# Kernel tuning notes

Hardware: AMD Instinct MI355X
Metric: run time of the kernel (lower is better)

## Reference

```python
import jax, jax.numpy as jnp
import numpy as np

NUM_WORDS = 256  # max word index + 1 (sentinel row NUM_WORDS used to drop non-first-occurrence scatters)


def setup_inputs() -> dict:
    key = jax.random.key(0)
    ks = jax.random.split(key, 8)
    B, S, H, R, D, C = 16, 512, 768, 8, 512, 27
    hidden_states = jax.random.normal(ks[0], (B, S, H), jnp.float32)
    word_ids = jnp.sort(jax.random.randint(ks[1], (B, S), 0, NUM_WORDS), axis=-1)
    relations_positions = jax.random.randint(ks[2], (B, R), 0, S)
    w_rel = jax.random.normal(ks[3], (H,), jnp.float32) / np.sqrt(H).astype(np.float32)
    b_rel = jnp.zeros((1,), jnp.float32)
    w1 = jax.random.normal(ks[4], (2 * H, D), jnp.float32) / np.sqrt(2 * H).astype(np.float32)
    b1 = jnp.zeros((D,), jnp.float32)
    w2 = jax.random.normal(ks[5], (D, C), jnp.float32) / np.sqrt(D).astype(np.float32)
    b2 = jnp.zeros((C,), jnp.float32)
    return dict(hidden_states=hidden_states, word_ids=word_ids,
                relations_positions=relations_positions,
                w_rel=w_rel, b_rel=b_rel, w1=w1, b1=b1, w2=w2, b2=b2)


def reference(hidden_states, word_ids, relations_positions, w_rel, b_rel, w1, b1, w2, b2):
    B, S, H = hidden_states.shape
    # relational logits: Linear(H, 1).squeeze(-1)  -> [B, S]
    rel_logits = jnp.einsum('bsh,h->bs', hidden_states, w_rel) + b_rel

    # first_hidden_states[i, w] = hidden_states[i, j] at the FIRST token j of word w
    # (torch loop keys on word_id != prev_word_id; word_ids are monotone per row)
    first_occ = jnp.concatenate(
        [jnp.ones((B, 1), bool), word_ids[:, 1:] != word_ids[:, :-1]], axis=1)
    tgt = jnp.where(first_occ, word_ids, NUM_WORDS)  # route non-first tokens to sentinel row
    batch_idx = jnp.arange(B)[:, None]
    first_hidden = (jnp.zeros((B, NUM_WORDS + 1, H), hidden_states.dtype)
                    .at[batch_idx, tgt].set(hidden_states))[:, :NUM_WORDS]  # [B, W, H]

    # gather relation token embeddings -> [B, R, H]
    rel_hidden = jnp.take_along_axis(
        hidden_states, relations_positions[:, :, None], axis=1)

    # concat([word_embed, rel_embed]) @ w1 == word_embed @ w1[:H] + rel_embed @ w1[H:]
    h_word = jnp.einsum('bwh,hd->bwd', first_hidden, w1[:H])   # [B, W, D]
    h_rel = jnp.einsum('brh,hd->brd', rel_hidden, w1[H:])      # [B, R, D]
    hmid = jax.nn.relu(h_word[:, None, :, :] + h_rel[:, :, None, :] + b1)  # [B, R, W, D]
    role_logits = jnp.einsum('brwd,dc->brwc', hmid, w2) + b2   # [B, R, W, C]

    return rel_logits, role_logits
```

## Files before the change

### kernel.cpp

```cpp
#include <hip/hip_runtime.h>
#include <hip/hip_bf16.h>

#define BB 16
#define SS 512
#define HH 768
#define RR 8
#define DD 512
#define CC 27
#define WW 256

typedef __attribute__((ext_vector_type(8))) short short8;
typedef __attribute__((ext_vector_type(4))) float f32x4;

union PKu { unsigned short us[8]; uint4 u4; short8 s8; };

__device__ __forceinline__ unsigned short f32_to_bf16_rne(float v) {
    unsigned int u = __float_as_uint(v);
    unsigned int r = u + 0x7fffu + ((u >> 16) & 1u);
    return (unsigned short)(r >> 16);
}
__device__ __forceinline__ float bf16_to_f32(unsigned short u) {
    return __uint_as_float(((unsigned int)u) << 16);
}

__device__ __forceinline__ void glds16(const void* g, void* l) {
    __builtin_amdgcn_global_load_lds(
        (const __attribute__((address_space(1))) unsigned int*)g,
        (__attribute__((address_space(3))) unsigned int*)l, 16, 0, 0);
}


__global__ __launch_bounds__(256) void k_front(
    const float* __restrict__ hidden, const int* __restrict__ word_ids,
    const int* __restrict__ relpos, const float4* __restrict__ wrel4,
    const float* __restrict__ b_rel, const float* __restrict__ w1,
    const float* __restrict__ w2, float* __restrict__ out0,
    unsigned short* __restrict__ first_hidden,
    unsigned short* __restrict__ rel_hidden,
    unsigned short* __restrict__ w1t, unsigned short* __restrict__ w2t) {
    int bid = blockIdx.x, t = threadIdx.x;
    if (bid < 2048) {
        int lane = t & 63;
        int row = bid * 4 + (t >> 6);
        const float4* hid4 = (const float4*)hidden + (size_t)row * (HH / 4);
        float4 v[3];
        float acc = 0.f;
#pragma unroll
        for (int j = 0; j < 3; ++j) {
            v[j] = hid4[j * 64 + lane];
            float4 w = wrel4[j * 64 + lane];
            acc += v[j].x * w.x + v[j].y * w.y + v[j].z * w.z + v[j].w * w.w;
        }
#pragma unroll
        for (int off = 32; off > 0; off >>= 1) acc += __shfl_xor(acc, off, 64);
        if (lane == 0) out0[row] = acc + b_rel[0];
        int wid = word_ids[row];
        int s = row & (SS - 1);
        int prev = (s == 0) ? -1 : word_ids[row - 1];
        if (wid != prev) {
            int b = row >> 9;
            unsigned short* dst = first_hidden + (size_t)(b * WW + wid) * HH;
#pragma unroll
            for (int j = 0; j < 3; ++j) {
                union { unsigned short us[4]; uint2 u2; } pk;
                pk.us[0] = f32_to_bf16_rne(v[j].x);
                pk.us[1] = f32_to_bf16_rne(v[j].y);
                pk.us[2] = f32_to_bf16_rne(v[j].z);
                pk.us[3] = f32_to_bf16_rne(v[j].w);
                *(uint2*)(dst + j * 256 + lane * 4) = pk.u2;
            }
        }
        return;
    }
    int x = bid - 2048;
    if (x < 192) {
        __shared__ unsigned short tile[64][72];
        int kt = x >> 3, nt = x & 7;
        int i = t >> 2, j4 = (t & 3) * 16;
        const float* src = w1 + (size_t)(kt * 64 + i) * DD + nt * 64 + j4;
#pragma unroll
        for (int v = 0; v < 4; ++v) {
            float4 f = *(const float4*)(src + v * 4);
            tile[i][j4 + v * 4 + 0] = f32_to_bf16_rne(f.x);
            tile[i][j4 + v * 4 + 1] = f32_to_bf16_rne(f.y);
            tile[i][j4 + v * 4 + 2] = f32_to_bf16_rne(f.z);
            tile[i][j4 + v * 4 + 3] = f32_to_bf16_rne(f.w);
        }
        __syncthreads();
        int jj = t >> 2, cb = (t & 3) * 16;
        union { unsigned short us[16]; uint4 u4[2]; } ov;
#pragma unroll
        for (int v = 0; v < 16; ++v) ov.us[v] = tile[cb + v][jj];
        unsigned short* dst = w1t + (size_t)(nt * 64 + jj) * (2 * HH) + kt * 64 + cb;
        *(uint4*)(dst) = ov.u4[0];
        *(uint4*)(dst + 8) = ov.u4[1];
    } else if (x == 192) {
        for (int idx = t; idx < 32 * DD; idx += 256) {
            int n = idx >> 9, k = idx & (DD - 1);
            float v = (n < CC) ? w2[(size_t)k * CC + n] : 0.f;
            w2t[n * DD + k] = f32_to_bf16_rne(v);
        }
    } else {
        __shared__ int pres[WW];
        int b = x - 193;
        pres[t] = 0;
        __syncthreads();
        for (int s = t; s < SS; s += 256) pres[word_ids[b * SS + s]] = 1;
        __syncthreads();
        if (!pres[t]) {
            uint4 z = {0u, 0u, 0u, 0u};
            unsigned short* dst = first_hidden + (size_t)(b * WW + t) * HH;
#pragma unroll 4
            for (int c = 0; c < 96; ++c) *(uint4*)(dst + c * 8) = z;
        }
        for (int idx = t; idx < 1024; idx += 256) {
            int rr = idx >> 7, c = idx & 127;
            if (c < 96) {
                int pos = relpos[b * RR + rr];
                const float* srow = hidden + (size_t)(b * SS + pos) * HH + c * 8;
                PKu pk;
#pragma unroll
                for (int e = 0; e < 8; ++e) pk.us[e] = f32_to_bf16_rne(srow[e]);
                *(uint4*)(rel_hidden + (size_t)(b * RR + rr) * HH + c * 8) = pk.u4;
            }
        }
    }
}

__global__ __launch_bounds__(256) void k_gemm(
    const unsigned short* __restrict__ first_hidden,
    const unsigned short* __restrict__ rel_hidden,
    const unsigned short* __restrict__ w1t,
    unsigned short* __restrict__ h_word, unsigned short* __restrict__ h_rel) {
    __shared__ __align__(16) unsigned char a_s[32768];
    __shared__ __align__(16) unsigned char b_s[32768];
    int nt = blockIdx.x;
    int mt = blockIdx.y;
    const unsigned short* A;
    unsigned short* C;
    int kbase, m0;
    if (mt < 64) { A = first_hidden; C = h_word; kbase = 0;  m0 = mt * 64; }
    else         { A = rel_hidden;   C = h_rel;  kbase = HH; m0 = (mt - 64) * 64; }
    int t = threadIdx.x;
    int wv = t >> 6, lane = t & 63;
    int wr = wv >> 1, wc = wv & 1;
    int q = lane >> 4, r = lane & 15;

    const unsigned char* aP[4];
    const unsigned char* bP[4];
    unsigned lofs[4];
#pragma unroll
    for (int j = 0; j < 4; ++j) {
        int ci = j * 256 + t;
        int row = ci >> 4, ch = ci & 15;
        int sc = ch ^ (row & 7);
        aP[j] = (const unsigned char*)A + (size_t)(m0 + row) * (HH * 2) + sc * 16;
        bP[j] = (const unsigned char*)w1t + (size_t)(nt * 64 + row) * (2 * HH * 2)
                + (size_t)kbase * 2 + sc * 16;
        lofs[j] = ci * 16;
    }
    f32x4 acc[2][2];
#pragma unroll
    for (int mi = 0; mi < 2; ++mi)
#pragma unroll
        for (int ni = 0; ni < 2; ++ni) acc[mi][ni] = (f32x4){0.f, 0.f, 0.f, 0.f};

#pragma unroll
    for (int j = 0; j < 4; ++j) glds16(aP[j], a_s + lofs[j]);
#pragma unroll
    for (int j = 0; j < 4; ++j) glds16(bP[j], b_s + lofs[j]);
    __syncthreads();

#pragma unroll
    for (int kt = 0; kt < 6; ++kt) {
        if (kt < 5) {
            unsigned nb = ((kt + 1) & 1) * 16384;
#pragma unroll
            for (int j = 0; j < 4; ++j) glds16(aP[j] + (kt + 1) * 256, a_s + nb + lofs[j]);
#pragma unroll
            for (int j = 0; j < 4; ++j) glds16(bP[j] + (kt + 1) * 256, b_s + nb + lofs[j]);
        }
        unsigned bo = (kt & 1) * 16384;
#pragma unroll
        for (int ks = 0; ks < 4; ++ks) {
            int c = ks * 4 + q;
            short8 bfr[2];
#pragma unroll
            for (int ni = 0; ni < 2; ++ni) {
                int row = wc * 32 + ni * 16 + r;
                bfr[ni] = *(const short8*)(b_s + bo + row * 256 + ((c ^ (row & 7)) << 4));
            }
#pragma unroll
            for (int mi = 0; mi < 2; ++mi) {
                int row = wr * 32 + mi * 16 + r;
                short8 af = *(const short8*)(a_s + bo + row * 256 + ((c ^ (row & 7)) << 4));
                acc[mi][0] = __builtin_amdgcn_mfma_f32_16x16x32_bf16(
                    af, bfr[0], acc[mi][0], 0, 0, 0);
                acc[mi][1] = __builtin_amdgcn_mfma_f32_16x16x32_bf16(
                    af, bfr[1], acc[mi][1], 0, 0, 0);
            }
        }
        __syncthreads();
    }
#pragma unroll
    for (int mi = 0; mi < 2; ++mi) {
        int m = m0 + wr * 32 + mi * 16 + q * 4;
#pragma unroll
        for (int ni = 0; ni < 2; ++ni) {
            int n = nt * 64 + wc * 32 + ni * 16 + r;
#pragma unroll
            for (int reg = 0; reg < 4; ++reg)
                C[(size_t)(m + reg) * DD + n] = f32_to_bf16_rne(acc[mi][ni][reg]);
        }
    }
}

__global__ __launch_bounds__(512) void k_role(
    const unsigned short* __restrict__ h_word, const unsigned short* __restrict__ h_rel,
    const unsigned short* __restrict__ w2t, const float* __restrict__ b1,
    const float* __restrict__ b2, float* __restrict__ out_role) {
    int wt = blockIdx.x;
    int b  = blockIdx.y;
    int t  = threadIdx.x;
    __shared__ __align__(16) unsigned char hw_s[32768];
    __shared__ float hr_s[RR][DD];
    __shared__ __align__(16) unsigned char w2_s[32768];
    {
        int wl = t >> 5;
        int cb = (t & 31) * 4;
        const unsigned short* srcr = h_word + (size_t)(b * WW + wt * 16 + wl) * DD;
        unsigned wlx = (wl & 7) << 4;
#pragma unroll
        for (int i = 0; i < 4; ++i) {
            int c = cb + i;
            uint2 hv = *(const uint2*)(srcr + c * 4);
            float4 bv = *(const float4*)(b1 + c * 4);
            float4 o;
            o.x = bf16_to_f32((unsigned short)(hv.x & 0xffffu)) + bv.x;
            o.y = bf16_to_f32((unsigned short)(hv.x >> 16)) + bv.y;
            o.z = bf16_to_f32((unsigned short)(hv.y & 0xffffu)) + bv.z;
            o.w = bf16_to_f32((unsigned short)(hv.y >> 16)) + bv.w;
            *(float4*)(hw_s + wl * 2048 + ((unsigned)(c * 16) ^ wlx)) = o;
        }
    }
    {
        int rr = t >> 6, cc = (t & 63) * 8;
        PKu hv;
        hv.u4 = *(const uint4*)(h_rel + (size_t)(b * RR + rr) * DD + cc);
        float4 o0, o1;
        o0.x = bf16_to_f32(hv.us[0]); o0.y = bf16_to_f32(hv.us[1]);
        o0.z = bf16_to_f32(hv.us[2]); o0.w = bf16_to_f32(hv.us[3]);
        o1.x = bf16_to_f32(hv.us[4]); o1.y = bf16_to_f32(hv.us[5]);
        o1.z = bf16_to_f32(hv.us[6]); o1.w = bf16_to_f32(hv.us[7]);
        *(float4*)&hr_s[rr][cc]     = o0;
        *(float4*)&hr_s[rr][cc + 4] = o1;
    }
    {
        int n = t >> 4, cb = (t & 15) * 4;
        unsigned nx = (n & 7) << 4;
        const unsigned short* srcw = w2t + n * DD + cb * 8;
#pragma unroll
        for (int i = 0; i < 4; ++i)
            *(uint4*)(w2_s + n * 1024 + ((unsigned)((cb + i) * 16) ^ nx)) =
                *(const uint4*)(srcw + i * 8);
    }
    __syncthreads();
    int wv = t >> 6, lane = t & 63, q = lane >> 4, wl = lane & 15;
    int rr = wv;
    unsigned wlx = (wl & 7) << 4;
    f32x4 acc[2];
#pragma unroll
    for (int ni = 0; ni < 2; ++ni) acc[ni] = (f32x4){0.f, 0.f, 0.f, 0.f};

    for (int ks = 0; ks < DD / 32; ++ks) {
        int k0 = ks * 32;
        short8 bfr[2];
#pragma unroll
        for (int ni = 0; ni < 2; ++ni) {
            int n = ni * 16 + wl;
            bfr[ni] = *(const short8*)(w2_s + n * 1024 +
                        ((unsigned)((4 * ks + q) * 16) ^ wlx));
        }
        int c0 = 8 * ks + 2 * q;
        float4 f0 = *(const float4*)(hw_s + wl * 2048 + ((unsigned)(c0 * 16) ^ wlx));
        float4 f1 = *(const float4*)(hw_s + wl * 2048 + ((unsigned)((c0 + 1) * 16) ^ wlx));
        const float* hrp = &hr_s[rr][k0 + 8 * q];
        float4 h0 = *(const float4*)(hrp);
        float4 h1 = *(const float4*)(hrp + 4);
        PKu pk;
        pk.us[0] = f32_to_bf16_rne(fmaxf(f0.x + h0.x, 0.f));
        pk.us[1] = f32_to_bf16_rne(fmaxf(f0.y + h0.y, 0.f));
        pk.us[2] = f32_to_bf16_rne(fmaxf(f0.z + h0.z, 0.f));
        pk.us[3] = f32_to_bf16_rne(fmaxf(f0.w + h0.w, 0.f));
        pk.us[4] = f32_to_bf16_rne(fmaxf(f1.x + h1.x, 0.f));
        pk.us[5] = f32_to_bf16_rne(fmaxf(f1.y + h1.y, 0.f));
        pk.us[6] = f32_to_bf16_rne(fmaxf(f1.z + h1.z, 0.f));
        pk.us[7] = f32_to_bf16_rne(fmaxf(f1.w + h1.w, 0.f));
#pragma unroll
        for (int ni = 0; ni < 2; ++ni)
            acc[ni] = __builtin_amdgcn_mfma_f32_16x16x32_bf16(
                pk.s8, bfr[ni], acc[ni], 0, 0, 0);
    }
#pragma unroll
    for (int ni = 0; ni < 2; ++ni) {
        int c = ni * 16 + wl;
        if (c < CC) {
#pragma unroll
            for (int reg = 0; reg < 4; ++reg) {
                int wg = wt * 16 + 4 * q + reg;
                out_role[(size_t)((b * RR + rr) * WW + wg) * CC + c] =
                    acc[ni][reg] + b2[c];
            }
        }
    }
}

extern "C" void kernel_launch(void* const* d_in, const int* in_sizes, int n_in,
                              void* d_out, int out_size, void* d_ws, size_t ws_size,
                              hipStream_t stream) {
    const float* hidden   = (const float*)d_in[0];
    const int*   word_ids = (const int*)d_in[1];
    const int*   relpos   = (const int*)d_in[2];
    const float* w_rel    = (const float*)d_in[3];
    const float* b_rel    = (const float*)d_in[4];
    const float* w1       = (const float*)d_in[5];
    const float* b1       = (const float*)d_in[6];
    const float* w2       = (const float*)d_in[7];
    const float* b2       = (const float*)d_in[8];

    float* out0 = (float*)d_out;
    float* out1 = out0 + BB * SS;

    unsigned short* first_hidden = (unsigned short*)d_ws;
    unsigned short* rel_hidden   = (unsigned short*)((char*)d_ws + 6291456);
    unsigned short* w1t          = (unsigned short*)((char*)d_ws + 6488064);
    unsigned short* w2t          = (unsigned short*)((char*)d_ws + 8060928);
    unsigned short* h_word       = (unsigned short*)((char*)d_ws + 8093696);
    unsigned short* h_rel        = (unsigned short*)((char*)d_ws + 12288000);

    k_front<<<2048 + 209, 256, 0, stream>>>(
        hidden, word_ids, relpos, (const float4*)w_rel, b_rel, w1, w2,
        out0, first_hidden, rel_hidden, w1t, w2t);
    k_gemm<<<dim3(8, 66), 256, 0, stream>>>(
        first_hidden, rel_hidden, w1t, h_word, h_rel);
    k_role<<<dim3(WW / 16, BB), 512, 0, stream>>>(h_word, h_rel, w2t, b1, b2, out1);
}
```

Measured before the change: 46.52 us.

## Enlarge GEMM M-tile, fold b1 into GEMM epilogue, async-load role tiles

The word-projection GEMM now uses 128-row M tiles with a 64-wide K step. This halves the grid and doubles A-tile reuse of each B tile. The b1 bias is added in the GEMM epilogue instead of in k_role, so k_role can keep h_word as bf16 in shared memory and stage it and w2 with direct global-to-LDS loads rather than converting through registers. The trade-off is fewer blocks (264), which may underfill the GPU, and twice as many K iterations with more syncs.

```diff
diff --git a/kernel.cpp b/kernel.cpp
--- a/kernel.cpp
+++ b/kernel.cpp
@@ -130,70 +130,83 @@
 __global__ __launch_bounds__(256) void k_gemm(
     const unsigned short* __restrict__ first_hidden,
     const unsigned short* __restrict__ rel_hidden,
-    const unsigned short* __restrict__ w1t,
+    const unsigned short* __restrict__ w1t, const float* __restrict__ b1,
     unsigned short* __restrict__ h_word, unsigned short* __restrict__ h_rel) {
     __shared__ __align__(16) unsigned char a_s[32768];
-    __shared__ __align__(16) unsigned char b_s[32768];
+    __shared__ __align__(16) unsigned char b_s[16384];
     int nt = blockIdx.x;
     int mt = blockIdx.y;
-    const unsigned short* A;
-    unsigned short* C;
-    int kbase, m0;
-    if (mt < 64) { A = first_hidden; C = h_word; kbase = 0;  m0 = mt * 64; }
-    else         { A = rel_hidden;   C = h_rel;  kbase = HH; m0 = (mt - 64) * 64; }
+    bool isw = (mt < 32);
+    const unsigned short* A = isw ? first_hidden : rel_hidden;
+    unsigned short* C = isw ? h_word : h_rel;
+    int kbase = isw ? 0 : HH;
+    int m0 = isw ? mt * 128 : 0;
     int t = threadIdx.x;
     int wv = t >> 6, lane = t & 63;
     int wr = wv >> 1, wc = wv & 1;
     int q = lane >> 4, r = lane & 15;
 
     const unsigned char* aP[4];
-    const unsigned char* bP[4];
-    unsigned lofs[4];
+    const unsigned char* bP[2];
+    unsigned lofa[4], lofb[2];
 #pragma unroll
     for (int j = 0; j < 4; ++j) {
         int ci = j * 256 + t;
-        int row = ci >> 4, ch = ci & 15;
+        int row = ci >> 3, ch = ci & 7;
         int sc = ch ^ (row & 7);
         aP[j] = (const unsigned char*)A + (size_t)(m0 + row) * (HH * 2) + sc * 16;
+        lofa[j] = ci * 16;
+    }
+#pragma unroll
+    for (int j = 0; j < 2; ++j) {
+        int ci = j * 256 + t;
+        int row = ci >> 3, ch = ci & 7;
+        int sc = ch ^ (row & 7);
         bP[j] = (const unsigned char*)w1t + (size_t)(nt * 64 + row) * (2 * HH * 2)
                 + (size_t)kbase * 2 + sc * 16;
-        lofs[j] = ci * 16;
-    }
-    f32x4 acc[2][2];
-#pragma unroll
-    for (int mi = 0; mi < 2; ++mi)
+        lofb[j] = ci * 16;
+    }
+    int arow[4], brow[2];
+#pragma unroll
+    for (int mi = 0; mi < 4; ++mi) arow[mi] = wr * 64 + mi * 16 + r;
+#pragma unroll
+    for (int ni = 0; ni < 2; ++ni) brow[ni] = wc * 32 + ni * 16 + r;
+
+    f32x4 acc[4][2];
+#pragma unroll
+    for (int mi = 0; mi < 4; ++mi)
 #pragma unroll
         for (int ni = 0; ni < 2; ++ni) acc[mi][ni] = (f32x4){0.f, 0.f, 0.f, 0.f};
 
 #pragma unroll
-    for (int j = 0; j < 4; ++j) glds16(aP[j], a_s + lofs[j]);
-#pragma unroll
-    for (int j = 0; j < 4; ++j) glds16(bP[j], b_s + lofs[j]);
+    for (int j = 0; j < 4; ++j) glds16(aP[j], a_s + lofa[j]);
+#pragma unroll
+    for (int j = 0; j < 2; ++j) glds16(bP[j], b_s + lofb[j]);
     __syncthreads();
 
-#pragma unroll
-    for (int kt = 0; kt < 6; ++kt) {
-        if (kt < 5) {
-            unsigned nb = ((kt + 1) & 1) * 16384;
-#pragma unroll
-            for (int j = 0; j < 4; ++j) glds16(aP[j] + (kt + 1) * 256, a_s + nb + lofs[j]);
-#pragma unroll
-            for (int j = 0; j < 4; ++j) glds16(bP[j] + (kt + 1) * 256, b_s + nb + lofs[j]);
-        }
-        unsigned bo = (kt & 1) * 16384;
-#pragma unroll
-        for (int ks = 0; ks < 4; ++ks) {
+    for (int kt = 0; kt < 12; ++kt) {
+        if (kt < 11) {
+            unsigned na = ((kt + 1) & 1) * 16384;
+            unsigned nb = ((kt + 1) & 1) * 8192;
+#pragma unroll
+            for (int j = 0; j < 4; ++j) glds16(aP[j] + (kt + 1) * 128, a_s + na + lofa[j]);
+#pragma unroll
+            for (int j = 0; j < 2; ++j) glds16(bP[j] + (kt + 1) * 128, b_s + nb + lofb[j]);
+        }
+        unsigned ba = (kt & 1) * 16384;
+        unsigned bb = (kt & 1) * 8192;
+#pragma unroll
+        for (int ks = 0; ks < 2; ++ks) {
             int c = ks * 4 + q;
             short8 bfr[2];
 #pragma unroll
-            for (int ni = 0; ni < 2; ++ni) {
-                int row = wc * 32 + ni * 16 + r;
-                bfr[ni] = *(const short8*)(b_s + bo + row * 256 + ((c ^ (row & 7)) << 4));
-            }
-#pragma unroll
-            for (int mi = 0; mi < 2; ++mi) {
-                int row = wr * 32 + mi * 16 + r;
-                short8 af = *(const short8*)(a_s + bo + row * 256 + ((c ^ (row & 7)) << 4));
+            for (int ni = 0; ni < 2; ++ni)
+                bfr[ni] = *(const short8*)(b_s + bb + brow[ni] * 128 +
+                            ((c ^ (brow[ni] & 7)) << 4));
+#pragma unroll
+            for (int mi = 0; mi < 4; ++mi) {
+                short8 af = *(const short8*)(a_s + ba + arow[mi] * 128 +
+                            ((c ^ (arow[mi] & 7)) << 4));
                 acc[mi][0] = __builtin_amdgcn_mfma_f32_16x16x32_bf16(
                     af, bfr[0], acc[mi][0], 0, 0, 0);
                 acc[mi][1] = __builtin_amdgcn_mfma_f32_16x16x32_bf16(
@@ -202,100 +215,97 @@
         }
         __syncthreads();
     }
-#pragma unroll
-    for (int mi = 0; mi < 2; ++mi) {
-        int m = m0 + wr * 32 + mi * 16 + q * 4;
+    float bias[2];
+#pragma unroll
+    for (int ni = 0; ni < 2; ++ni) {
+        int n = nt * 64 + wc * 32 + ni * 16 + r;
+        bias[ni] = isw ? b1[n] : 0.f;
+    }
+#pragma unroll
+    for (int mi = 0; mi < 4; ++mi) {
+        int m = m0 + wr * 64 + mi * 16 + q * 4;
 #pragma unroll
         for (int ni = 0; ni < 2; ++ni) {
             int n = nt * 64 + wc * 32 + ni * 16 + r;
 #pragma unroll
             for (int reg = 0; reg < 4; ++reg)
-                C[(size_t)(m + reg) * DD + n] = f32_to_bf16_rne(acc[mi][ni][reg]);
+                C[(size_t)(m + reg) * DD + n] =
+                    f32_to_bf16_rne(acc[mi][ni][reg] + bias[ni]);
         }
     }
 }
 
 __global__ __launch_bounds__(512) void k_role(
     const unsigned short* __restrict__ h_word, const unsigned short* __restrict__ h_rel,
-    const unsigned short* __restrict__ w2t, const float* __restrict__ b1,
-    const float* __restrict__ b2, float* __restrict__ out_role) {
+    const unsigned short* __restrict__ w2t, const float* __restrict__ b2,
+    float* __restrict__ out_role) {
     int wt = blockIdx.x;
     int b  = blockIdx.y;
     int t  = threadIdx.x;
-    __shared__ __align__(16) unsigned char hw_s[32768];
+    __shared__ __align__(16) unsigned char hw_s[16384];
     __shared__ float hr_s[RR][DD];
     __shared__ __align__(16) unsigned char w2_s[32768];
+    int wv = t >> 6, lane = t & 63;
     {
-        int wl = t >> 5;
-        int cb = (t & 31) * 4;
-        const unsigned short* srcr = h_word + (size_t)(b * WW + wt * 16 + wl) * DD;
-        unsigned wlx = (wl & 7) << 4;
+#pragma unroll
+        for (int i = 0; i < 2; ++i) {
+            int row = wv * 2 + i;
+            const unsigned short* src = h_word +
+                (size_t)(b * WW + wt * 16 + row) * DD + ((lane ^ (row & 7)) * 8);
+            glds16(src, hw_s + row * 1024 + lane * 16);
+        }
+    }
+    {
 #pragma unroll
         for (int i = 0; i < 4; ++i) {
-            int c = cb + i;
-            uint2 hv = *(const uint2*)(srcr + c * 4);
-            float4 bv = *(const float4*)(b1 + c * 4);
-            float4 o;
-            o.x = bf16_to_f32((unsigned short)(hv.x & 0xffffu)) + bv.x;
-            o.y = bf16_to_f32((unsigned short)(hv.x >> 16)) + bv.y;
-            o.z = bf16_to_f32((unsigned short)(hv.y & 0xffffu)) + bv.z;
-            o.w = bf16_to_f32((unsigned short)(hv.y >> 16)) + bv.w;
-            *(float4*)(hw_s + wl * 2048 + ((unsigned)(c * 16) ^ wlx)) = o;
+            int row = wv * 4 + i;
+            const unsigned short* src = w2t + row * DD + ((lane ^ (row & 7)) * 8);
+            glds16(src, w2_s + row * 1024 + lane * 16);
         }
     }
     {
-        int rr = t >> 6, cc = (t & 63) * 8;
+        int rr = t >> 6, c = t & 63;
         PKu hv;
-        hv.u4 = *(const uint4*)(h_rel + (size_t)(b * RR + rr) * DD + cc);
+        hv.u4 = *(const uint4*)(h_rel + (size_t)(b * RR + rr) * DD + c * 8);
         float4 o0, o1;
         o0.x = bf16_to_f32(hv.us[0]); o0.y = bf16_to_f32(hv.us[1]);
         o0.z = bf16_to_f32(hv.us[2]); o0.w = bf16_to_f32(hv.us[3]);
         o1.x = bf16_to_f32(hv.us[4]); o1.y = bf16_to_f32(hv.us[5]);
         o1.z = bf16_to_f32(hv.us[6]); o1.w = bf16_to_f32(hv.us[7]);
-        *(float4*)&hr_s[rr][cc]     = o0;
-        *(float4*)&hr_s[rr][cc + 4] = o1;
-    }
-    {
-        int n = t >> 4, cb = (t & 15) * 4;
-        unsigned nx = (n & 7) << 4;
-        const unsigned short* srcw = w2t + n * DD + cb * 8;
-#pragma unroll
-        for (int i = 0; i < 4; ++i)
-            *(uint4*)(w2_s + n * 1024 + ((unsigned)((cb + i) * 16) ^ nx)) =
-                *(const uint4*)(srcw + i * 8);
+        *(float4*)&hr_s[rr][c * 8]     = o0;
+        *(float4*)&hr_s[rr][c * 8 + 4] = o1;
     }
     __syncthreads();
-    int wv = t >> 6, lane = t & 63, q = lane >> 4, wl = lane & 15;
+    int q = lane >> 4, wl = lane & 15;
     int rr = wv;
     unsigned wlx = (wl & 7) << 4;
     f32x4 acc[2];
 #pragma unroll
     for (int ni = 0; ni < 2; ++ni) acc[ni] = (f32x4){0.f, 0.f, 0.f, 0.f};
 
+#pragma unroll 2
     for (int ks = 0; ks < DD / 32; ++ks) {
-        int k0 = ks * 32;
+        int c = 4 * ks + q;
         short8 bfr[2];
 #pragma unroll
         for (int ni = 0; ni < 2; ++ni) {
             int n = ni * 16 + wl;
-            bfr[ni] = *(const short8*)(w2_s + n * 1024 +
-                        ((unsigned)((4 * ks + q) * 16) ^ wlx));
-        }
-        int c0 = 8 * ks + 2 * q;
-        float4 f0 = *(const float4*)(hw_s + wl * 2048 + ((unsigned)(c0 * 16) ^ wlx));
-        float4 f1 = *(const float4*)(hw_s + wl * 2048 + ((unsigned)((c0 + 1) * 16) ^ wlx));
-        const float* hrp = &hr_s[rr][k0 + 8 * q];
+            bfr[ni] = *(const short8*)(w2_s + n * 1024 + ((c ^ (n & 7)) << 4));
+        }
+        PKu hw;
+        hw.u4 = *(const uint4*)(hw_s + wl * 1024 + ((unsigned)(c << 4) ^ wlx));
+        const float* hrp = &hr_s[rr][ks * 32 + q * 8];
         float4 h0 = *(const float4*)(hrp);
         float4 h1 = *(const float4*)(hrp + 4);
         PKu pk;
-        pk.us[0] = f32_to_bf16_rne(fmaxf(f0.x + h0.x, 0.f));
-        pk.us[1] = f32_to_bf16_rne(fmaxf(f0.y + h0.y, 0.f));
-        pk.us[2] = f32_to_bf16_rne(fmaxf(f0.z + h0.z, 0.f));
-        pk.us[3] = f32_to_bf16_rne(fmaxf(f0.w + h0.w, 0.f));
-        pk.us[4] = f32_to_bf16_rne(fmaxf(f1.x + h1.x, 0.f));
-        pk.us[5] = f32_to_bf16_rne(fmaxf(f1.y + h1.y, 0.f));
-        pk.us[6] = f32_to_bf16_rne(fmaxf(f1.z + h1.z, 0.f));
-        pk.us[7] = f32_to_bf16_rne(fmaxf(f1.w + h1.w, 0.f));
+        pk.us[0] = f32_to_bf16_rne(fmaxf(bf16_to_f32(hw.us[0]) + h0.x, 0.f));
+        pk.us[1] = f32_to_bf16_rne(fmaxf(bf16_to_f32(hw.us[1]) + h0.y, 0.f));
+        pk.us[2] = f32_to_bf16_rne(fmaxf(bf16_to_f32(hw.us[2]) + h0.z, 0.f));
+        pk.us[3] = f32_to_bf16_rne(fmaxf(bf16_to_f32(hw.us[3]) + h0.w, 0.f));
+        pk.us[4] = f32_to_bf16_rne(fmaxf(bf16_to_f32(hw.us[4]) + h1.x, 0.f));
+        pk.us[5] = f32_to_bf16_rne(fmaxf(bf16_to_f32(hw.us[5]) + h1.y, 0.f));
+        pk.us[6] = f32_to_bf16_rne(fmaxf(bf16_to_f32(hw.us[6]) + h1.z, 0.f));
+        pk.us[7] = f32_to_bf16_rne(fmaxf(bf16_to_f32(hw.us[7]) + h1.w, 0.f));
 #pragma unroll
         for (int ni = 0; ni < 2; ++ni)
             acc[ni] = __builtin_amdgcn_mfma_f32_16x16x32_bf16(
@@ -341,7 +351,7 @@
     k_front<<<2048 + 209, 256, 0, stream>>>(
         hidden, word_ids, relpos, (const float4*)w_rel, b_rel, w1, w2,
         out0, first_hidden, rel_hidden, w1t, w2t);
-    k_gemm<<<dim3(8, 66), 256, 0, stream>>>(
-        first_hidden, rel_hidden, w1t, h_word, h_rel);
-    k_role<<<dim3(WW / 16, BB), 512, 0, stream>>>(h_word, h_rel, w2t, b1, b2, out1);
-}
+    k_gemm<<<dim3(8, 33), 256, 0, stream>>>(
+        first_hidden, rel_hidden, w1t, b1, h_word, h_rel);
+    k_role<<<dim3(WW / 16, BB), 512, 0, stream>>>(h_word, h_rel, w2t, b2, out1);
+}
```

New measurement: 44.59 us. -4.2%, faster.
